# Kernel tuning notes

Hardware: AMD Instinct MI355X
Metric: run time of the kernel (lower is better)

## Reference

```python
import jax, jax.numpy as jnp
import numpy as np
from jax import lax

P = 16          # patch size
C = 1024        # embed dim
NH = 8          # heads
HD = C // NH    # head dim = 128


def setup_inputs() -> dict:
    key = jax.random.key(0)
    ks = jax.random.split(key, 12)
    B = 64
    s = 0.02
    return {
        "x": jax.random.normal(ks[0], (B, 1, 256, 256), jnp.float32),
        "conv_w": jax.random.normal(ks[1], (C, 1, P, P), jnp.float32) * s,
        "conv_b": jnp.zeros((C,), jnp.float32),
        "Wq": jax.random.normal(ks[2], (C, C), jnp.float32) * s,
        "bq": jnp.zeros((C,), jnp.float32),
        "Wk": jax.random.normal(ks[3], (C, C), jnp.float32) * s,
        "bk": jnp.zeros((C,), jnp.float32),
        "Wv": jax.random.normal(ks[4], (C, C), jnp.float32) * s,
        "bv": jnp.zeros((C,), jnp.float32),
        "Wp": jax.random.normal(ks[5], (C, C), jnp.float32) * s,
        "bp": jnp.zeros((C,), jnp.float32),
    }


def _forward(x, conv_w, conv_b, Wq, bq, Wk, bk, Wv, bv, Wp, bp):
    # PatchEmbed: 16x16 stride-16 conv -> [B, C, 16, 16]
    h = lax.conv_general_dilated(
        x, conv_w, window_strides=(P, P), padding="VALID",
        dimension_numbers=("NCHW", "OIHW", "NCHW"))
    h = h + conv_b[None, :, None, None]
    B = h.shape[0]
    T = h.shape[2] * h.shape[3]  # 256
    tok = h.reshape(B, C, T).transpose(0, 2, 1)  # [B, T, C]

    def heads(W, b):
        y = jnp.einsum("btc,cd->btd", tok, W) + b
        return y.reshape(B, T, NH, HD).transpose(0, 2, 1, 3)  # [B, H, T, D]

    q, k, v = heads(Wq, bq), heads(Wk, bk), heads(Wv, bv)
    present = jnp.stack((k, v))  # [2, B, H, T, D]

    att = jnp.einsum("bhqd,bhkd->bhqk", q, k) * (1.0 / np.sqrt(HD))
    causal = jnp.tril(jnp.ones((T, T), bool))
    att = jnp.where(causal[None, None], att, -jnp.inf)
    att = jax.nn.softmax(att, axis=-1)  # dropout: eval mode (identity)

    y = jnp.einsum("bhqk,bhkd->bhqd", att, v)
    y = y.transpose(0, 2, 1, 3).reshape(B, T, C)
    y = jnp.einsum("btc,cd->btd", y, Wp) + bp  # resid dropout: identity
    return y, present


def reference(x, conv_w, conv_b, Wq, bq, Wk, bk, Wv, bv, Wp, bp):
    return _forward(x, conv_w, conv_b, Wq, bq, Wk, bk, Wv, bv, Wp, bp)
```

## Files before the change

### kernel.cpp

```cpp
#include <hip/hip_runtime.h>


typedef unsigned short u16;
typedef unsigned int u32;
typedef __attribute__((ext_vector_type(8))) short bf16x8;
typedef __attribute__((ext_vector_type(4))) float f32x4;
typedef __attribute__((ext_vector_type(4))) u16 u16x4;

#define Y_ELEMS  16777216
#define KV_ELEMS 16777216

__device__ __forceinline__ u16 f2b(float f) {
  u32 u = __float_as_uint(f);
  u32 r = u + 0x7fffu + ((u >> 16) & 1u);
  return (u16)(r >> 16);
}

__device__ __forceinline__ float b2f(u16 h) {
  return __uint_as_float(((u32)h) << 16);
}

__device__ __forceinline__ void gl_lds16(const u16* g, u16* l) {
  __builtin_amdgcn_global_load_lds(
      (__attribute__((address_space(1))) void*)g,
      (__attribute__((address_space(3))) void*)l, 16, 0, 0);
}

__global__ __launch_bounds__(256) void patchify_kernel(
    const float* __restrict__ x, u16* __restrict__ ap) {
  int tid = blockIdx.x * 256 + threadIdx.x;
  float4 v = ((const float4*)x)[tid];
  int col4 = tid & 63;
  int row  = (tid >> 6) & 255;
  int b    = tid >> 14;
  int py = row >> 4, ky = row & 15;
  int col = col4 << 2;
  int px = col >> 4, kx = col & 15;
  size_t dst = ((size_t)(b * 256 + py * 16 + px)) * 256 + ky * 16 + kx;
  u16x4 o = { f2b(v.x), f2b(v.y), f2b(v.z), f2b(v.w) };
  *(u16x4*)(ap + dst) = o;
}

__global__ __launch_bounds__(256) void transpose_wc_kernel(
    const float* __restrict__ W, u16* __restrict__ o) {
  __shared__ float tile[32][33];
  int x0 = blockIdx.x * 32, y0 = blockIdx.y * 32;
  int tx = threadIdx.x, ty = threadIdx.y;
#pragma unroll
  for (int i = ty; i < 32; i += 8)
    tile[i][tx] = W[(size_t)(y0 + i) * 256 + x0 + tx];
  __syncthreads();
#pragma unroll
  for (int i = ty; i < 32; i += 8)
    o[(size_t)(x0 + i) * 1024 + y0 + tx] = f2b(tile[tx][i]);
}

__global__ __launch_bounds__(256) void transpose_w_kernel(
    const float* __restrict__ Wq, const float* __restrict__ Wk,
    const float* __restrict__ Wv, const float* __restrict__ Wp,
    u16* __restrict__ Wqkv_t, u16* __restrict__ Wp_t) {
  __shared__ float tile[32][33];
  int z = blockIdx.z;
  const float* W = (z == 0) ? Wq : (z == 1) ? Wk : (z == 2) ? Wv : Wp;
  u16* dst = (z < 3) ? (Wqkv_t + (size_t)z * 1024 * 1024) : Wp_t;
  int x0 = blockIdx.x * 32, y0 = blockIdx.y * 32;
  int tx = threadIdx.x, ty = threadIdx.y;
#pragma unroll
  for (int i = ty; i < 32; i += 8)
    tile[i][tx] = W[(size_t)(y0 + i) * 1024 + x0 + tx];
  __syncthreads();
#pragma unroll
  for (int i = ty; i < 32; i += 8)
    dst[(size_t)(x0 + i) * 1024 + y0 + tx] = f2b(tile[tx][i]);
}

__global__ __launch_bounds__(256) void bias_fold_kernel(
    const u16* __restrict__ Wqkv_t, const float* __restrict__ conv_b,
    const float* __restrict__ bq, const float* __restrict__ bk,
    const float* __restrict__ bv, float* __restrict__ bias_f) {
  int lane = threadIdx.x & 63, w = threadIdx.x >> 6;
  int n = blockIdx.x * 4 + w;
  const u16* row = Wqkv_t + (size_t)n * 1024 + lane * 16;
  const float* cb = conv_b + lane * 16;
  bf16x8 a0 = *(const bf16x8*)row;
  bf16x8 a1 = *(const bf16x8*)(row + 8);
  float s = 0.f;
#pragma unroll
  for (int e = 0; e < 8; ++e) s += b2f((u16)a0[e]) * cb[e];
#pragma unroll
  for (int e = 0; e < 8; ++e) s += b2f((u16)a1[e]) * cb[8 + e];
#pragma unroll
  for (int off = 1; off < 64; off <<= 1) s += __shfl_xor(s, off, 64);
  if (lane == 0) {
    int seg = n >> 10, j = n & 1023;
    float base = (seg == 0 ? bq : seg == 1 ? bk : bv)[j];
    bias_f[n] = base + s;
  }
}

__global__ __launch_bounds__(256) void gemm_kernel(
    const u16* __restrict__ A, const u16* __restrict__ Bt,
    int K, int N, int mode, const float* __restrict__ bias0,
    u16* __restrict__ ob0, u16* __restrict__ ob1, u16* __restrict__ ob2,
    float* __restrict__ of0) {
  __shared__ __attribute__((aligned(16))) char smem[17408];
  u16* As = (u16*)smem;
  u16* Bs = (u16*)(smem + 8192);
  const int t = threadIdx.x;
  const int rr = t >> 2;
  const int c8 = (t & 3) << 3;
  const int lane = t & 63;
  const int w = t >> 6;
  const int wm = (w & 1) << 6, wn = (w >> 1) << 6;
  const int l15 = lane & 15, quad = lane >> 4;
  const int tile_m = blockIdx.x * 128, tile_n = blockIdx.y * 128;

  f32x4 acc[4][4];
  f32x4 zero = {0.f, 0.f, 0.f, 0.f};
#pragma unroll
  for (int i = 0; i < 4; ++i)
#pragma unroll
    for (int j = 0; j < 4; ++j) acc[i][j] = zero;

  const u16* gA0 = A + (size_t)(tile_m + rr) * K + c8;
  const u16* gA1 = A + (size_t)(tile_m + 64 + rr) * K + c8;
  const u16* gB0 = Bt + (size_t)(tile_n + rr) * K + c8;
  const u16* gB1 = Bt + (size_t)(tile_n + 64 + rr) * K + c8;
  u16* lA0 = As + rr * 32 + c8;
  u16* lA1 = As + (64 + rr) * 32 + c8;
  u16* lB0 = Bs + rr * 32 + c8;
  u16* lB1 = Bs + (64 + rr) * 32 + c8;

  for (int k0 = 0; k0 < K; k0 += 32) {
    __syncthreads();
    gl_lds16(gA0 + k0, lA0);
    gl_lds16(gA1 + k0, lA1);
    gl_lds16(gB0 + k0, lB0);
    gl_lds16(gB1 + k0, lB1);
    __syncthreads();
    bf16x8 af[4], bfr[4];
#pragma unroll
    for (int i = 0; i < 4; ++i)
      af[i] = *(const bf16x8*)(As + (wm + 16 * i + l15) * 32 + quad * 8);
#pragma unroll
    for (int j = 0; j < 4; ++j)
      bfr[j] = *(const bf16x8*)(Bs + (wn + 16 * j + l15) * 32 + quad * 8);
#pragma unroll
    for (int i = 0; i < 4; ++i)
#pragma unroll
      for (int j = 0; j < 4; ++j)
        acc[i][j] = __builtin_amdgcn_mfma_f32_16x16x32_bf16(af[i], bfr[j], acc[i][j], 0, 0, 0);
  }

  __syncthreads();
  float* ep = (float*)smem + w * 1088;
  const int ncol = wn + quad * 16;

  f32x4 ba[4];
  if (bias0) {
#pragma unroll
    for (int c = 0; c < 4; ++c)
      ba[c] = *(const f32x4*)(bias0 + tile_n + ncol + c * 4);
  } else {
#pragma unroll
    for (int c = 0; c < 4; ++c) ba[c] = zero;
  }

  int seg = 0, h = 0, dd = 0;
  u16* ob = ob0;
  float* pf = of0;
  if (mode == 1) {
    seg = tile_n >> 10;
    ob = (seg == 0) ? ob0 : (seg == 1) ? ob1 : ob2;
    pf = of0 + (size_t)(seg ? (seg - 1) : 0) * KV_ELEMS;
    int nloc = (tile_n & 1023) + ncol;
    h = nloc >> 7;
    dd = nloc & 127;
  }

#pragma unroll
  for (int i = 0; i < 4; ++i) {
#pragma unroll
    for (int j = 0; j < 4; ++j)
#pragma unroll
      for (int r = 0; r < 4; ++r)
        ep[(quad * 4 + r) * 68 + j * 16 + l15] = acc[i][j][r];
    asm volatile("s_waitcnt lgkmcnt(0)" ::: "memory");
    f32x4 vt[4];
#pragma unroll
    for (int c = 0; c < 4; ++c) {
      vt[c] = *(const f32x4*)(ep + l15 * 68 + quad * 16 + c * 4);
      vt[c] += ba[c];
    }
    asm volatile("s_waitcnt lgkmcnt(0)" ::: "memory");
    const int m = tile_m + wm + 16 * i + l15;

    bf16x8 h0, h1;
#pragma unroll
    for (int e = 0; e < 8; ++e) h0[e] = (short)f2b(vt[e >> 2][e & 3]);
#pragma unroll
    for (int e = 0; e < 8; ++e) h1[e] = (short)f2b(vt[2 + (e >> 2)][e & 3]);

    if (mode == 1) {
      int bb = m >> 8, tt = m & 255;
      size_t idx = ((size_t)(bb * 8 + h) * 256 + tt) * 128 + dd;
      *(bf16x8*)(ob + idx) = h0;
      *(bf16x8*)(ob + idx + 8) = h1;
      if (seg) {
#pragma unroll
        for (int c = 0; c < 4; ++c) *(f32x4*)(pf + idx + c * 4) = vt[c];
      }
    } else if (mode == 2) {
      float* p = of0 + (size_t)m * N + tile_n + ncol;
#pragma unroll
      for (int c = 0; c < 4; ++c) *(f32x4*)(p + c * 4) = vt[c];
    } else {
      u16* p = ob0 + (size_t)m * N + tile_n + ncol;
      *(bf16x8*)p = h0;
      *(bf16x8*)(p + 8) = h1;
    }
  }
}

__global__ __launch_bounds__(256) void attn_kernel(
    const u16* __restrict__ qw, const u16* __restrict__ kw,
    const u16* __restrict__ vw, u16* __restrict__ yatt) {
  __shared__ __attribute__((aligned(16))) u16 Ks[64 * 136];
  __shared__ __attribute__((aligned(16))) u16 Vs[128 * 72];
  __shared__ __attribute__((aligned(16))) u16 Ps[4 * 16 * 72];
  const int qb = blockIdx.x;
  const int bh = blockIdx.y;
  const int t = threadIdx.x;
  const int lane = t & 63, w = t >> 6;
  const int l15 = lane & 15, quad = lane >> 4;
  const int qrow0 = qb * 64 + w * 16;

  bf16x8 aq[4];
#pragma unroll
  for (int ks = 0; ks < 4; ++ks)
    aq[ks] = *(const bf16x8*)(qw + ((size_t)bh * 256 + qrow0 + l15) * 128 + ks * 32 + quad * 8);

  f32x4 o[8];
  f32x4 zero = {0.f, 0.f, 0.f, 0.f};
#pragma unroll
  for (int dt = 0; dt < 8; ++dt) o[dt] = zero;
  float mi[4] = {-1e30f, -1e30f, -1e30f, -1e30f};
  float li[4] = {0.f, 0.f, 0.f, 0.f};

  const int jp = (t & 31) * 2;
  const int db = (t >> 5) * 16;

  for (int j = 0; j <= qb; ++j) {
    __syncthreads();
    {
      const u16* ksrc = kw + ((size_t)bh * 256 + j * 64) * 128;
      int kr = t >> 2, kc = t & 3;
#pragma unroll
      for (int s = 0; s < 4; ++s) {
        int cb = s * 4 + kc;
        *(bf16x8*)(Ks + kr * 136 + cb * 8) = *(const bf16x8*)(ksrc + kr * 128 + cb * 8);
      }
      const u16* vsrc = vw + ((size_t)bh * 256 + j * 64) * 128;
      bf16x8 r0a = *(const bf16x8*)(vsrc + (size_t)jp * 128 + db);
      bf16x8 r0b = *(const bf16x8*)(vsrc + (size_t)jp * 128 + db + 8);
      bf16x8 r1a = *(const bf16x8*)(vsrc + (size_t)(jp + 1) * 128 + db);
      bf16x8 r1b = *(const bf16x8*)(vsrc + (size_t)(jp + 1) * 128 + db + 8);
#pragma unroll
      for (int dv = 0; dv < 8; ++dv) {
        u32 p = (u32)(u16)r0a[dv] | ((u32)(u16)r1a[dv] << 16);
        *(u32*)(Vs + (db + dv) * 72 + jp) = p;
      }
#pragma unroll
      for (int dv = 0; dv < 8; ++dv) {
        u32 p = (u32)(u16)r0b[dv] | ((u32)(u16)r1b[dv] << 16);
        *(u32*)(Vs + (db + 8 + dv) * 72 + jp) = p;
      }
    }
    __syncthreads();

    f32x4 s4[4];
#pragma unroll
    for (int nt = 0; nt < 4; ++nt) s4[nt] = zero;
#pragma unroll
    for (int nt = 0; nt < 4; ++nt)
#pragma unroll
      for (int ks = 0; ks < 4; ++ks) {
        bf16x8 bk8 = *(const bf16x8*)(Ks + (nt * 16 + l15) * 136 + ks * 32 + quad * 8);
        s4[nt] = __builtin_amdgcn_mfma_f32_16x16x32_bf16(aq[ks], bk8, s4[nt], 0, 0, 0);
      }

    const float sc = 0.08838834764831845f;
    const bool diag = (j == qb);
#pragma unroll
    for (int nt = 0; nt < 4; ++nt) {
      int coln = j * 64 + nt * 16 + l15;
#pragma unroll
      for (int r = 0; r < 4; ++r) {
        float sv = s4[nt][r] * sc;
        if (diag && coln > (qrow0 + quad * 4 + r)) sv = -1e30f;
        s4[nt][r] = sv;
      }
    }

#pragma unroll
    for (int r = 0; r < 4; ++r) {
      float mx = fmaxf(fmaxf(s4[0][r], s4[1][r]), fmaxf(s4[2][r], s4[3][r]));
#pragma unroll
      for (int off = 1; off < 16; off <<= 1)
        mx = fmaxf(mx, __shfl_xor(mx, off, 64));
      float mnew = fmaxf(mi[r], mx);
      float alpha = __expf(mi[r] - mnew);
      float sum = 0.f;
#pragma unroll
      for (int nt = 0; nt < 4; ++nt) {
        float p = __expf(s4[nt][r] - mnew);
        s4[nt][r] = p;
        sum += p;
      }
#pragma unroll
      for (int off = 1; off < 16; off <<= 1)
        sum += __shfl_xor(sum, off, 64);
      li[r] = li[r] * alpha + sum;
      mi[r] = mnew;
#pragma unroll
      for (int dt = 0; dt < 8; ++dt) o[dt][r] *= alpha;
    }

    u16* pw = Ps + w * 16 * 72;
#pragma unroll
    for (int nt = 0; nt < 4; ++nt)
#pragma unroll
      for (int r = 0; r < 4; ++r)
        pw[(quad * 4 + r) * 72 + nt * 16 + l15] = f2b(s4[nt][r]);
    asm volatile("s_waitcnt lgkmcnt(0)" ::: "memory");

    bf16x8 ap[2];
#pragma unroll
    for (int k2 = 0; k2 < 2; ++k2)
      ap[k2] = *(const bf16x8*)(pw + l15 * 72 + k2 * 32 + quad * 8);
#pragma unroll
    for (int dt = 0; dt < 8; ++dt)
#pragma unroll
      for (int k2 = 0; k2 < 2; ++k2) {
        bf16x8 bv8 = *(const bf16x8*)(Vs + (dt * 16 + l15) * 72 + k2 * 32 + quad * 8);
        o[dt] = __builtin_amdgcn_mfma_f32_16x16x32_bf16(ap[k2], bv8, o[dt], 0, 0, 0);
      }
  }

  const int b = bh >> 3, h = bh & 7;
#pragma unroll
  for (int r = 0; r < 4; ++r) {
    float inv = 1.0f / li[r];
    int tt = qrow0 + quad * 4 + r;
    size_t rowbase = ((size_t)b * 256 + tt) * 1024 + h * 128;
#pragma unroll
    for (int dt = 0; dt < 8; ++dt)
      yatt[rowbase + dt * 16 + l15] = f2b(o[dt][r] * inv);
  }
}

extern "C" void kernel_launch(void* const* d_in, const int* in_sizes, int n_in,
                              void* d_out, int out_size, void* d_ws, size_t ws_size,
                              hipStream_t stream) {
  const float* x      = (const float*)d_in[0];
  const float* conv_w = (const float*)d_in[1];
  const float* conv_b = (const float*)d_in[2];
  const float* Wq     = (const float*)d_in[3];
  const float* bq     = (const float*)d_in[4];
  const float* Wk     = (const float*)d_in[5];
  const float* bk     = (const float*)d_in[6];
  const float* Wv     = (const float*)d_in[7];
  const float* bv     = (const float*)d_in[8];
  const float* Wp     = (const float*)d_in[9];
  const float* bp     = (const float*)d_in[10];
  float* out = (float*)d_out;

  char* ws = (char*)d_ws;
  u16*   A_patch = (u16*)(ws);
  u16*   Wc_t    = (u16*)(ws + (8u << 20));
  u16*   W2      = (u16*)(ws + (8u << 20) + (1u << 19));
  float* bias_f  = (float*)(ws + (10u << 20));
  u16*   Wqkv_t  = (u16*)(ws + (10u << 20) + (1u << 16));
  u16*   y_att   = (u16*)(ws);
  u16*   Wp_t    = (u16*)(ws + (32u << 20));
  u16*   q_ws    = (u16*)(ws + (34u << 20));
  u16*   k_ws    = (u16*)(ws + (66u << 20));
  u16*   v_ws    = (u16*)(ws + (98u << 20));

  patchify_kernel<<<4096, 256, 0, stream>>>(x, A_patch);
  transpose_wc_kernel<<<dim3(8, 32), dim3(32, 8), 0, stream>>>(conv_w, Wc_t);
  transpose_w_kernel<<<dim3(32, 32, 4), dim3(32, 8), 0, stream>>>(
      Wq, Wk, Wv, Wp, Wqkv_t, Wp_t);
  bias_fold_kernel<<<768, 256, 0, stream>>>(Wqkv_t, conv_b, bq, bk, bv, bias_f);
  gemm_kernel<<<dim3(24, 2), 256, 0, stream>>>(
      Wqkv_t, Wc_t, 1024, 256, 0, nullptr,
      W2, nullptr, nullptr, nullptr);
  gemm_kernel<<<dim3(128, 24), 256, 0, stream>>>(
      A_patch, W2, 256, 3072, 1, bias_f,
      q_ws, k_ws, v_ws, out + Y_ELEMS);
  attn_kernel<<<dim3(4, 512), 256, 0, stream>>>(q_ws, k_ws, v_ws, y_att);
  gemm_kernel<<<dim3(128, 8), 256, 0, stream>>>(
      y_att, Wp_t, 1024, 1024, 2, bp,
      nullptr, nullptr, nullptr, out);
}
```

Before: 464.4 us.

## Prefetch next K/V tile into registers, remap attention grid, raise MFMA priority

The attention kernel now issues global loads for the next K/V tile into registers before computing on the current tile, then writes them to LDS after the PV matmul, so global latency can overlap with compute. The launch grid becomes 1D with a block-id remap that spreads consecutive blocks across bh values, which may improve XCD/L2 locality and load balance of causal blocks. s_setprio is raised around the MFMA loops. This costs extra registers for the staged tiles, which may reduce occupancy.

```diff
diff --git a/kernel.cpp b/kernel.cpp
--- a/kernel.cpp
+++ b/kernel.cpp
@@ -228,8 +228,11 @@
   __shared__ __attribute__((aligned(16))) u16 Ks[64 * 136];
   __shared__ __attribute__((aligned(16))) u16 Vs[128 * 72];
   __shared__ __attribute__((aligned(16))) u16 Ps[4 * 16 * 72];
-  const int qb = blockIdx.x;
-  const int bh = blockIdx.y;
+  const int id = blockIdx.x;
+  const int xr = id & 7;
+  const int kk = id >> 3;
+  const int qb = kk & 3;
+  const int bh = ((kk >> 2) << 3) + xr;
   const int t = threadIdx.x;
   const int lane = t & 63, w = t >> 6;
   const int l15 = lane & 15, quad = lane >> 4;
@@ -249,38 +252,51 @@
 
   const int jp = (t & 31) * 2;
   const int db = (t >> 5) * 16;
+  const int kr = t >> 2, kc = t & 3;
+  const u16* kbase = kw + (size_t)bh * 256 * 128;
+  const u16* vbase = vw + (size_t)bh * 256 * 128;
+
+  bf16x8 kreg[4], vr0a, vr0b, vr1a, vr1b;
+
+  auto stage_load = [&](int jt) {
+    const u16* ksrc = kbase + (size_t)jt * 64 * 128;
+#pragma unroll
+    for (int s = 0; s < 4; ++s)
+      kreg[s] = *(const bf16x8*)(ksrc + kr * 128 + (s * 4 + kc) * 8);
+    const u16* vsrc = vbase + (size_t)jt * 64 * 128;
+    vr0a = *(const bf16x8*)(vsrc + (size_t)jp * 128 + db);
+    vr0b = *(const bf16x8*)(vsrc + (size_t)jp * 128 + db + 8);
+    vr1a = *(const bf16x8*)(vsrc + (size_t)(jp + 1) * 128 + db);
+    vr1b = *(const bf16x8*)(vsrc + (size_t)(jp + 1) * 128 + db + 8);
+  };
+  auto stage_write = [&]() {
+#pragma unroll
+    for (int s = 0; s < 4; ++s)
+      *(bf16x8*)(Ks + kr * 136 + (s * 4 + kc) * 8) = kreg[s];
+#pragma unroll
+    for (int dv = 0; dv < 8; ++dv) {
+      u32 p = (u32)(u16)vr0a[dv] | ((u32)(u16)vr1a[dv] << 16);
+      *(u32*)(Vs + (db + dv) * 72 + jp) = p;
+    }
+#pragma unroll
+    for (int dv = 0; dv < 8; ++dv) {
+      u32 p = (u32)(u16)vr0b[dv] | ((u32)(u16)vr1b[dv] << 16);
+      *(u32*)(Vs + (db + 8 + dv) * 72 + jp) = p;
+    }
+  };
+
+  stage_load(0);
+  stage_write();
+  __syncthreads();
 
   for (int j = 0; j <= qb; ++j) {
-    __syncthreads();
-    {
-      const u16* ksrc = kw + ((size_t)bh * 256 + j * 64) * 128;
-      int kr = t >> 2, kc = t & 3;
-#pragma unroll
-      for (int s = 0; s < 4; ++s) {
-        int cb = s * 4 + kc;
-        *(bf16x8*)(Ks + kr * 136 + cb * 8) = *(const bf16x8*)(ksrc + kr * 128 + cb * 8);
-      }
-      const u16* vsrc = vw + ((size_t)bh * 256 + j * 64) * 128;
-      bf16x8 r0a = *(const bf16x8*)(vsrc + (size_t)jp * 128 + db);
-      bf16x8 r0b = *(const bf16x8*)(vsrc + (size_t)jp * 128 + db + 8);
-      bf16x8 r1a = *(const bf16x8*)(vsrc + (size_t)(jp + 1) * 128 + db);
-      bf16x8 r1b = *(const bf16x8*)(vsrc + (size_t)(jp + 1) * 128 + db + 8);
-#pragma unroll
-      for (int dv = 0; dv < 8; ++dv) {
-        u32 p = (u32)(u16)r0a[dv] | ((u32)(u16)r1a[dv] << 16);
-        *(u32*)(Vs + (db + dv) * 72 + jp) = p;
-      }
-#pragma unroll
-      for (int dv = 0; dv < 8; ++dv) {
-        u32 p = (u32)(u16)r0b[dv] | ((u32)(u16)r1b[dv] << 16);
-        *(u32*)(Vs + (db + 8 + dv) * 72 + jp) = p;
-      }
-    }
-    __syncthreads();
+    const bool more = (j < qb);
+    if (more) stage_load(j + 1);
 
     f32x4 s4[4];
 #pragma unroll
     for (int nt = 0; nt < 4; ++nt) s4[nt] = zero;
+    __builtin_amdgcn_s_setprio(1);
 #pragma unroll
     for (int nt = 0; nt < 4; ++nt)
 #pragma unroll
@@ -288,6 +304,7 @@
         bf16x8 bk8 = *(const bf16x8*)(Ks + (nt * 16 + l15) * 136 + ks * 32 + quad * 8);
         s4[nt] = __builtin_amdgcn_mfma_f32_16x16x32_bf16(aq[ks], bk8, s4[nt], 0, 0, 0);
       }
+    __builtin_amdgcn_s_setprio(0);
 
     const float sc = 0.08838834764831845f;
     const bool diag = (j == qb);
@@ -338,6 +355,7 @@
 #pragma unroll
     for (int k2 = 0; k2 < 2; ++k2)
       ap[k2] = *(const bf16x8*)(pw + l15 * 72 + k2 * 32 + quad * 8);
+    __builtin_amdgcn_s_setprio(1);
 #pragma unroll
     for (int dt = 0; dt < 8; ++dt)
 #pragma unroll
@@ -345,6 +363,13 @@
         bf16x8 bv8 = *(const bf16x8*)(Vs + (dt * 16 + l15) * 72 + k2 * 32 + quad * 8);
         o[dt] = __builtin_amdgcn_mfma_f32_16x16x32_bf16(ap[k2], bv8, o[dt], 0, 0, 0);
       }
+    __builtin_amdgcn_s_setprio(0);
+
+    __syncthreads();
+    if (more) {
+      stage_write();
+      __syncthreads();
+    }
   }
 
   const int b = bh >> 3, h = bh & 7;
@@ -398,7 +423,7 @@
   gemm_kernel<<<dim3(128, 24), 256, 0, stream>>>(
       A_patch, W2, 256, 3072, 1, bias_f,
       q_ws, k_ws, v_ws, out + Y_ELEMS);
-  attn_kernel<<<dim3(4, 512), 256, 0, stream>>>(q_ws, k_ws, v_ws, y_att);
+  attn_kernel<<<2048, 256, 0, stream>>>(q_ws, k_ws, v_ws, y_att);
   gemm_kernel<<<dim3(128, 8), 256, 0, stream>>>(
       y_att, Wp_t, 1024, 1024, 2, bp,
       nullptr, nullptr, nullptr, out);
```

After: 462.9 us. About the same (-0.3%).
